# Performance work log

Measured on AMD Instinct MI355X. Metric: run time of the kernel, lower is better.

Reference implementation:

```python
import jax, jax.numpy as jnp
import numpy as np

B, T, D, H, E, O, A = 8192, 223, 7, 128, 50, 29, 9
IMPUTE_W, LABEL_W = 0.3, 1.0

def setup_inputs() -> dict:
    key = jax.random.key(0)
    ks = jax.random.split(key, 32)
    u = lambda k, shape, fan: jax.random.uniform(k, shape, jnp.float32, -1.0/np.sqrt(fan), 1.0/np.sqrt(fan))
    return {
        'values':    jax.random.normal(ks[0], (B, T, D), jnp.float32),
        'masks':     (jax.random.uniform(ks[1], (B, T, D)) < 0.8).astype(jnp.float32),
        'deltas':    jax.random.uniform(ks[2], (B, T, D), jnp.float32) * 5.0,
        'probs':     jax.nn.softmax(jax.random.normal(ks[3], (B, O), jnp.float32), axis=1),
        'ancillary': jax.random.normal(ks[4], (B, A), jnp.float32),
        'labels':    jax.random.randint(ks[5], (B,), 0, O, jnp.int32),
        'W_td_h': u(ks[6], (H, D), H),  'b_td_h': u(ks[7], (H,), H),
        'W_td_x': u(ks[8], (D, D), D),  'b_td_x': u(ks[9], (D,), D),
        'W_hist': u(ks[10], (D, H), H), 'b_hist': u(ks[11], (D,), H),
        'W_feat': u(ks[12], (D, D), D), 'b_feat': u(ks[13], (D,), D),
        'W_comb': u(ks[14], (D, 2*D), 2*D), 'b_comb': u(ks[15], (D,), 2*D),
        'W_ih': u(ks[16], (4*H, 2*D), H), 'W_hh': u(ks[17], (4*H, H), H),
        'b_ih': u(ks[18], (4*H,), H),     'b_hh': u(ks[19], (4*H,), H),
        'W_anc': u(ks[20], (E, A), A),    'b_anc': u(ks[21], (E,), A),
        'W_cat': u(ks[22], (H, H + E), H + E), 'b_cat': u(ks[23], (H,), H + E),
        'W_out': u(ks[24], (O, H), H),    'b_out': u(ks[25], (O,), H),
    }

def _rits_forward(values, masks, deltas, probs, ancillary,
                  W_td_h, b_td_h, W_td_x, b_td_x, W_hist, b_hist,
                  W_feat, b_feat, W_comb, b_comb, W_ih, W_hh, b_ih, b_hh,
                  W_anc, b_anc, W_cat, b_cat, W_out, b_out):
    Bn = values.shape[0]
    td_x_diag = jnp.diag(W_td_x)                     # diag=True decay uses only diagonal
    Wf = W_feat * (1.0 - jnp.eye(D, dtype=W_feat.dtype))

    def step(carry, xt):
        h, c, xl = carry
        x, m, d = xt                                  # each [B, D]
        gamma_h = jnp.exp(-jax.nn.relu(d @ W_td_h.T + b_td_h))   # [B, H]
        gamma_x = jnp.exp(-jax.nn.relu(d * td_x_diag + b_td_x))  # [B, D]
        h = h * gamma_h
        x_h = h @ W_hist.T + b_hist
        msum = jnp.sum(m) + 1e-5
        xl = xl + jnp.sum(jnp.abs(x - x_h) * m) / msum
        x_c = m * x + (1.0 - m) * x_h
        z_h = x_c @ Wf.T + b_feat
        xl = xl + jnp.sum(jnp.abs(x - z_h) * m) / msum
        alpha = jnp.concatenate([gamma_x, m], axis=1) @ W_comb.T + b_comb
        c_h = alpha * z_h + (1.0 - alpha) * x_h
        xl = xl + jnp.sum(jnp.abs(x - c_h) * m) / msum
        c_c = m * x + (1.0 - m) * c_h
        inputs = jnp.concatenate([c_c, m], axis=1)    # [B, 2D]
        gates = inputs @ W_ih.T + b_ih + h @ W_hh.T + b_hh  # [B, 4H]
        i, f, g, o = jnp.split(gates, 4, axis=1)
        c = jax.nn.sigmoid(f) * c + jax.nn.sigmoid(i) * jnp.tanh(g)
        h = jax.nn.sigmoid(o) * jnp.tanh(c)
        return (h, c, xl), c_c

    h0 = jnp.zeros((Bn, H), values.dtype)
    c0 = jnp.zeros((Bn, H), values.dtype)
    xs = (jnp.swapaxes(values, 0, 1), jnp.swapaxes(masks, 0, 1), jnp.swapaxes(deltas, 0, 1))
    (h, c, x_loss), imps = jax.lax.scan(step, (h0, c0, jnp.float32(0.0)), xs)
    imputations = jnp.swapaxes(imps, 0, 1)           # [B, T, D]

    x_loss = x_loss * IMPUTE_W
    anc = jax.nn.relu(ancillary @ W_anc.T + b_anc)
    h = jax.nn.relu(jnp.concatenate([h, anc], axis=1) @ W_cat.T + b_cat)
    y_h = jax.nn.softmax(h @ W_out.T + b_out, axis=1)
    y_loss = jnp.sum((y_h - probs) ** 2) / (Bn + 1e-5) * LABEL_W
    return x_loss, y_loss, x_loss + y_loss, y_h, imputations

def reference(values, masks, deltas, probs, ancillary, labels,
              W_td_h, b_td_h, W_td_x, b_td_x, W_hist, b_hist,
              W_feat, b_feat, W_comb, b_comb, W_ih, W_hh, b_ih, b_hh,
              W_anc, b_anc, W_cat, b_cat, W_out, b_out):
    x_loss, y_loss, loss, y_h, imputations = _rits_forward(
        values, masks, deltas, probs, ancillary,
        W_td_h, b_td_h, W_td_x, b_td_x, W_hist, b_hist,
        W_feat, b_feat, W_comb, b_comb, W_ih, W_hh, b_ih, b_hh,
        W_anc, b_anc, W_cat, b_cat, W_out, b_out)
    return (x_loss, y_loss, loss, y_h, imputations, labels)
```

## Files before the change

### kernel.cpp

```cpp
#include <hip/hip_runtime.h>
#include <math.h>

#define B_ 8192
#define T_ 223
#define D_ 7
#define H_ 128
#define G_ 512
#define E_ 50
#define O_ 29
#define A_ 9
#define TD_ (T_*D_)
#define NB 32
#define NTHR 512
#define MB 8

#define WS_MINV  0
#define WS_ACC   (WS_MINV + T_)
#define WS_WCATT (WS_ACC + 2)
#define WS_HFIN  (WS_WCATT + 178*H_)

#define OUT_YH  3
#define OUT_IMP (OUT_YH + B_*O_)
#define OUT_LAB (OUT_IMP + B_*T_*D_)

typedef __attribute__((ext_vector_type(8))) short short8;
typedef __attribute__((ext_vector_type(4))) float floatx4;
#define MFMA16(Av,Bv,Cv) __builtin_amdgcn_mfma_f32_16x16x32_bf16((Av),(Bv),(Cv),0,0,0)

__device__ __forceinline__ unsigned short f2bf(float f) {
    unsigned int u = __builtin_bit_cast(unsigned int, f);
    return (unsigned short)((u + 0x7FFFu + ((u >> 16) & 1u)) >> 16);
}
__device__ __forceinline__ float bf2f(unsigned short s) {
    unsigned int u = ((unsigned int)s) << 16;
    return __builtin_bit_cast(float, u);
}
__device__ __forceinline__ float rcp_(float x)  { return __builtin_amdgcn_rcpf(x); }
__device__ __forceinline__ float sigm(float x)  { return rcp_(1.f + __expf(-x)); }
__device__ __forceinline__ float tanh_(float x) { return 1.f - 2.f*rcp_(1.f + __expf(2.f*x)); }

__global__ void rits_prep(const float* __restrict__ W_cat, float* __restrict__ ws)
{
    int idx = blockIdx.x * 256 + threadIdx.x;
    if (idx < H_*178) {
        int j = idx / 178, k = idx - j*178;
        ws[WS_WCATT + k*H_ + j] = W_cat[idx];
    }
    if (idx < 2) ws[WS_ACC + idx] = 0.f;
}

__global__ void rits_msum(const float* __restrict__ masks, float* __restrict__ ws)
{
    const int t = blockIdx.x, tid = threadIdx.x;
    float s = 0.f;
    for (int i = tid; i < B_*D_; i += 256) {
        int b = i / D_, q = i - b*D_;
        s += masks[b*TD_ + t*D_ + q];
    }
    for (int off = 32; off > 0; off >>= 1) s += __shfl_down(s, off, 64);
    __shared__ float r[4];
    if ((tid & 63) == 0) r[tid >> 6] = s;
    __syncthreads();
    if (tid == 0) ws[WS_MINV + t] = 1.f / (r[0]+r[1]+r[2]+r[3] + 1e-5f);
}

__global__ __launch_bounds__(NTHR, 2) void rits_main(
    const float* __restrict__ values, const float* __restrict__ masks, const float* __restrict__ deltas,
    const float* __restrict__ W_td_h, const float* __restrict__ b_td_h,
    const float* __restrict__ W_td_x, const float* __restrict__ b_td_x,
    const float* __restrict__ W_hist, const float* __restrict__ b_hist,
    const float* __restrict__ W_feat, const float* __restrict__ b_feat,
    const float* __restrict__ W_comb, const float* __restrict__ b_comb,
    const float* __restrict__ W_ih, const float* __restrict__ W_hh,
    const float* __restrict__ b_ih, const float* __restrict__ b_hh,
    float* __restrict__ ws, float* __restrict__ out)
{
    __shared__ __attribute__((aligned(16))) unsigned short hbuf[NB*168];
    __shared__ __attribute__((aligned(16))) unsigned short dbuf[NB*72];
    __shared__ __attribute__((aligned(16))) unsigned short whis_lds[16*136];
    __shared__ float xs[NB*8], msh[NB*8], dsl[NB*8];
    __shared__ float xh_l[NB*8], xc_l[NB*8], gx_l[NB*8];
    __shared__ float bhist_l[8], tdx_l[8], btdx_l[8];
    __shared__ float impbuf[NB*16*7];
    __shared__ float red[8];

    const int tid  = threadIdx.x;
    const int b0   = blockIdx.x * NB;
    const int lane = tid & 63;
    const int w    = tid >> 6;
    const int quad = lane >> 4;
    const int l15  = lane & 15;

    for (int i = tid; i < NB*168; i += NTHR) hbuf[i] = 0;
    for (int i = tid; i < NB*72;  i += NTHR) dbuf[i] = 0;
    for (int i = tid; i < 16*136; i += NTHR) {
        int r = i / 136, c = i - r*136;
        whis_lds[i] = (r < 7 && c < 128) ? f2bf(W_hist[r*H_ + c]) : 0;
    }
    if (tid < 8) {
        bhist_l[tid] = (tid < 7) ? b_hist[tid] : 0.f;
        tdx_l[tid]   = (tid < 7) ? W_td_x[tid*D_ + tid] : 0.f;
        btdx_l[tid]  = (tid < 7) ? b_td_x[tid] : 0.f;
    }

    short8 whhf[4][4];
    short8 winf[4];
    short8 wtdf;
    float  biasg_r[4][4];
    float  btdh_r[4];
    {
        union UU { short8 v; unsigned short u[8]; } fr;
        #pragma unroll
        for (int c = 0; c < 4; ++c) {
            const int j = (c*8 + w)*16 + l15;
            #pragma unroll
            for (int s = 0; s < 4; ++s) {
                const float* p = W_hh + j*H_ + s*32 + quad*8;
                #pragma unroll
                for (int e = 0; e < 8; ++e) fr.u[e] = f2bf(p[e]);
                whhf[c][s] = fr.v;
            }
            #pragma unroll
            for (int e = 0; e < 8; ++e) {
                int k = quad*8 + e;
                fr.u[e] = (k < 14) ? f2bf(W_ih[j*14 + k]) : (unsigned short)0;
            }
            winf[c] = fr.v;
            #pragma unroll
            for (int r = 0; r < 4; ++r) {
                int jj = (c*8 + w)*16 + quad*4 + r;
                biasg_r[c][r] = b_ih[jj] + b_hh[jj];
            }
        }
        #pragma unroll
        for (int e = 0; e < 8; ++e) {
            int k = quad*8 + e;
            fr.u[e] = (k < 7) ? f2bf(W_td_h[(w*16 + l15)*D_ + k]) : (unsigned short)0;
        }
        wtdf = fr.v;
        #pragma unroll
        for (int r = 0; r < 4; ++r) btdh_r[r] = b_td_h[w*16 + quad*4 + r];
    }

    const bool ldr = (tid < NB*D_);
    const int  lb  = tid / D_, li = tid - (tid/D_)*D_;
    float wfr[7], wcr[14], bfr = 0.f, bcr = 0.f;
    if (ldr) {
        #pragma unroll
        for (int k = 0; k < 7; ++k)  wfr[k] = (k == li) ? 0.f : W_feat[li*D_ + k];
        #pragma unroll
        for (int k = 0; k < 14; ++k) wcr[k] = W_comb[li*14 + k];
        bfr = b_feat[li];  bcr = b_comb[li];
    }

    float c_st[2][4] = {{0,0,0,0},{0,0,0,0}};
    float lacc = 0.f;

    const long gbase = (long)(b0 + lb)*TD_ + li;
    float rx = 0.f, rm = 0.f, rd = 0.f;
    if (ldr) { rx = values[gbase]; rm = masks[gbase]; rd = deltas[gbase]; }

    const float* minv = ws + WS_MINV;

    for (int t = 0; t < T_; ++t) {
        if (ldr) { xs[lb*8+li] = rx; msh[lb*8+li] = rm; dsl[lb*8+li] = rd; }
        __syncthreads();
        if (ldr && t + 1 < T_) {
            const long g = gbase + (long)(t+1)*D_;
            rx = values[g]; rm = masks[g]; rd = deltas[g];
        }

        floatx4 acc[4][2];
        #pragma unroll
        for (int c = 0; c < 4; ++c)
            #pragma unroll
            for (int nt = 0; nt < 2; ++nt) {
                floatx4 a = { biasg_r[c][0], biasg_r[c][1], biasg_r[c][2], biasg_r[c][3] };
                acc[c][nt] = a;
            }
        floatx4 xh0 = {0,0,0,0}, xh1 = {0,0,0,0};
        #pragma unroll
        for (int s = 0; s < 4; ++s) {
            short8 hb0 = *(const short8*)&hbuf[l15*168       + s*32 + quad*8];
            short8 hb1 = *(const short8*)&hbuf[(16+l15)*168  + s*32 + quad*8];
            #pragma unroll
            for (int c = 0; c < 4; ++c) {
                acc[c][0] = MFMA16(whhf[c][s], hb0, acc[c][0]);
                acc[c][1] = MFMA16(whhf[c][s], hb1, acc[c][1]);
            }
            if (w == 7) {
                short8 wh = *(const short8*)&whis_lds[l15*136 + s*32 + quad*8];
                xh0 = MFMA16(wh, hb0, xh0);
                xh1 = MFMA16(wh, hb1, xh1);
            }
        }
        if (w == 7 && quad < 2) {
            #pragma unroll
            for (int nt = 0; nt < 2; ++nt) {
                const int b = nt*16 + l15;
                floatx4 xv = nt ? xh1 : xh0;
                #pragma unroll
                for (int r = 0; r < 4; ++r) {
                    const int i = quad*4 + r;
                    if (i < 7) {
                        float xhv = xv[r] + bhist_l[i];
                        float x = xs[b*8+i], m = msh[b*8+i], d = dsl[b*8+i];
                        xh_l[b*8+i] = xhv;
                        xc_l[b*8+i] = m*x + (1.f-m)*xhv;
                        gx_l[b*8+i] = __expf(-fmaxf(fmaf(d, tdx_l[i], btdx_l[i]), 0.f));
                    }
                }
            }
        }
        __syncthreads();

        if (ldr) {
            const int b = lb, i = li;
            const float invt = minv[t];
            const float x = xs[b*8+i], m = msh[b*8+i];
            float zh = bfr;
            #pragma unroll
            for (int k = 0; k < 7; ++k) zh = fmaf(wfr[k], xc_l[b*8+k], zh);
            float al = bcr;
            #pragma unroll
            for (int k = 0; k < 7; ++k) al = fmaf(wcr[k],   gx_l[b*8+k], al);
            #pragma unroll
            for (int k = 0; k < 7; ++k) al = fmaf(wcr[7+k], msh[b*8+k], al);
            const float xhv = xh_l[b*8+i];
            const float ch  = al*zh + (1.f-al)*xhv;
            const float cc  = m*x + (1.f-m)*ch;
            impbuf[(b*16 + (t & 15))*7 + i] = cc;
            hbuf[b*168 + 128 + i] = f2bf(cc);
            hbuf[b*168 + 135 + i] = f2bf(m);
            dbuf[b*72 + i] = f2bf(rd);
            lacc = fmaf((fabsf(x-xhv) + fabsf(x-zh) + fabsf(x-ch)) * m, invt, lacc);
        }
        __syncthreads();

        {
            short8 ib0 = *(const short8*)&hbuf[l15*168      + 128 + quad*8];
            short8 ib1 = *(const short8*)&hbuf[(16+l15)*168 + 128 + quad*8];
            #pragma unroll
            for (int c = 0; c < 4; ++c) {
                acc[c][0] = MFMA16(winf[c], ib0, acc[c][0]);
                acc[c][1] = MFMA16(winf[c], ib1, acc[c][1]);
            }
        }
        floatx4 g0 = {0,0,0,0}, g1 = {0,0,0,0};
        const bool dec = (t + 1 < T_);
        if (dec) {
            short8 df0 = *(const short8*)&dbuf[l15*72      + quad*8];
            short8 df1 = *(const short8*)&dbuf[(16+l15)*72 + quad*8];
            floatx4 z = {0,0,0,0};
            g0 = MFMA16(wtdf, df0, z);
            g1 = MFMA16(wtdf, df1, z);
        }
        #pragma unroll
        for (int nt = 0; nt < 2; ++nt) {
            const int b = nt*16 + l15;
            floatx4 gg = nt ? g1 : g0;
            #pragma unroll
            for (int r = 0; r < 4; ++r) {
                float ig = acc[0][nt][r], fg = acc[1][nt][r];
                float gv = acc[2][nt][r], og = acc[3][nt][r];
                float cn = sigm(fg)*c_st[nt][r] + sigm(ig)*tanh_(gv);
                c_st[nt][r] = cn;
                float hn = sigm(og)*tanh_(cn);
                if (dec) hn *= __expf(-fmaxf(gg[r] + btdh_r[r], 0.f));
                hbuf[b*168 + w*16 + quad*4 + r] = f2bf(hn);
            }
        }

        if ((t & 15) == 15 || t == T_ - 1) {
            const int t0 = t & ~15;
            const int b  = tid >> 4, c16 = tid & 15;
            if (t0 + c16 <= t) {
                float* gp = out + (size_t)OUT_IMP + (size_t)(b0+b)*TD_ + (size_t)(t0+c16)*D_;
                const float* lp = &impbuf[(b*16 + c16)*7];
                #pragma unroll
                for (int e = 0; e < 7; ++e) gp[e] = lp[e];
            }
        }
    }
    __syncthreads();

    for (int off = 32; off > 0; off >>= 1) lacc += __shfl_down(lacc, off, 64);
    if ((tid & 63) == 0) red[tid >> 6] = lacc;
    __syncthreads();
    if (tid == 0) {
        float s = 0.f;
        #pragma unroll
        for (int q = 0; q < 8; ++q) s += red[q];
        atomicAdd(&ws[WS_ACC], s);
    }
    for (int i = tid; i < NB*H_; i += NTHR) {
        int b = i >> 7, j = i & 127;
        ws[WS_HFIN + (size_t)(b0+b)*H_ + j] = bf2f(hbuf[b*168 + j]);
    }
}

__global__ __launch_bounds__(128) void rits_head(
    const float* __restrict__ probs, const float* __restrict__ ancillary, const int* __restrict__ labels,
    const float* __restrict__ W_anc, const float* __restrict__ b_anc,
    const float* __restrict__ b_cat,
    const float* __restrict__ W_out, const float* __restrict__ b_out,
    float* __restrict__ ws, float* __restrict__ out)
{
    __shared__ float hb[MB*H_];
    __shared__ float ancl[MB*52];
    __shared__ float hc[MB*H_];
    __shared__ float lg[MB*32];
    __shared__ float smx[MB], sinv[MB], ysum[MB];
    __shared__ float sq[MB*32];
    const int tid = threadIdx.x;
    const int bb0 = blockIdx.x * MB;

    for (int i = tid; i < MB*H_; i += 128) hb[i] = ws[WS_HFIN + (size_t)bb0*H_ + i];
    for (int i = tid; i < MB*E_; i += 128) {
        int b = i / E_, e = i - b*E_;
        float s = b_anc[e];
        #pragma unroll
        for (int a = 0; a < A_; ++a) s = fmaf(ancillary[(bb0+b)*A_ + a], W_anc[e*A_ + a], s);
        ancl[b*52+e] = fmaxf(s, 0.f);
    }
    __syncthreads();
    {
        const int j = tid;
        float s[MB];
        #pragma unroll
        for (int b = 0; b < MB; ++b) s[b] = b_cat[j];
        const float* wc = ws + WS_WCATT;
        for (int k = 0; k < H_; ++k) {
            float wv = wc[k*H_ + j];
            #pragma unroll
            for (int b = 0; b < MB; ++b) s[b] = fmaf(hb[b*H_+k], wv, s[b]);
        }
        for (int k = 0; k < E_; ++k) {
            float wv = wc[(H_+k)*H_ + j];
            #pragma unroll
            for (int b = 0; b < MB; ++b) s[b] = fmaf(ancl[b*52+k], wv, s[b]);
        }
        #pragma unroll
        for (int b = 0; b < MB; ++b) hc[b*H_+j] = fmaxf(s[b], 0.f);
    }
    __syncthreads();
    for (int i = tid; i < MB*O_; i += 128) {
        int b = i / O_, o = i - b*O_;
        float s = b_out[o];
        for (int k = 0; k < H_; ++k) s = fmaf(hc[b*H_+k], W_out[o*H_+k], s);
        lg[b*32+o] = s;
    }
    __syncthreads();
    if (tid < MB) {
        float mx = -1e30f;
        for (int o = 0; o < O_; ++o) mx = fmaxf(mx, lg[tid*32+o]);
        float se = 0.f;
        for (int o = 0; o < O_; ++o) se += __expf(lg[tid*32+o] - mx);
        smx[tid] = mx; sinv[tid] = 1.f / se;
    }
    __syncthreads();
    for (int i = tid; i < MB*O_; i += 128) {
        int b = i / O_, o = i - b*O_;
        float y = __expf(lg[b*32+o] - smx[b]) * sinv[b];
        out[OUT_YH + (size_t)(bb0+b)*O_ + o] = y;
        float d = y - probs[(size_t)(bb0+b)*O_ + o];
        sq[b*32+o] = d*d;
    }
    __syncthreads();
    if (tid < MB) {
        float s = 0.f;
        for (int o = 0; o < O_; ++o) s += sq[tid*32+o];
        ysum[tid] = s;
        out[OUT_LAB + bb0 + tid] = (float)labels[bb0 + tid];
    }
    __syncthreads();
    if (tid == 0) {
        float s = 0.f;
        #pragma unroll
        for (int b = 0; b < MB; ++b) s += ysum[b];
        atomicAdd(&ws[WS_ACC+1], s);
    }
}

__global__ void rits_fin(const float* __restrict__ ws, float* __restrict__ out)
{
    if (blockIdx.x == 0 && threadIdx.x == 0) {
        float xl = ws[WS_ACC] * 0.3f;
        float yl = ws[WS_ACC+1] * (1.0f / (8192.0f + 1e-5f));
        out[0] = xl; out[1] = yl; out[2] = xl + yl;
    }
}

extern "C" void kernel_launch(void* const* d_in, const int* in_sizes, int n_in,
                              void* d_out, int out_size, void* d_ws, size_t ws_size,
                              hipStream_t stream)
{
    const float* values = (const float*)d_in[0];
    const float* masks  = (const float*)d_in[1];
    const float* deltas = (const float*)d_in[2];
    const float* probs  = (const float*)d_in[3];
    const float* ancil  = (const float*)d_in[4];
    const int*   labels = (const int*)  d_in[5];
    const float* W_td_h = (const float*)d_in[6];
    const float* b_td_h = (const float*)d_in[7];
    const float* W_td_x = (const float*)d_in[8];
    const float* b_td_x = (const float*)d_in[9];
    const float* W_hist = (const float*)d_in[10];
    const float* b_hist = (const float*)d_in[11];
    const float* W_feat = (const float*)d_in[12];
    const float* b_feat = (const float*)d_in[13];
    const float* W_comb = (const float*)d_in[14];
    const float* b_comb = (const float*)d_in[15];
    const float* W_ih   = (const float*)d_in[16];
    const float* W_hh   = (const float*)d_in[17];
    const float* b_ih   = (const float*)d_in[18];
    const float* b_hh   = (const float*)d_in[19];
    const float* W_anc  = (const float*)d_in[20];
    const float* b_anc  = (const float*)d_in[21];
    const float* W_cat  = (const float*)d_in[22];
    const float* b_cat  = (const float*)d_in[23];
    const float* W_out  = (const float*)d_in[24];
    const float* b_out  = (const float*)d_in[25];
    float* ws  = (float*)d_ws;
    float* out = (float*)d_out;

    hipLaunchKernelGGL(rits_prep, dim3((H_*178 + 255)/256), dim3(256), 0, stream, W_cat, ws);
    hipLaunchKernelGGL(rits_msum, dim3(T_), dim3(256), 0, stream, masks, ws);
    hipLaunchKernelGGL(rits_main, dim3(B_/NB), dim3(NTHR), 0, stream,
                       values, masks, deltas, W_td_h, b_td_h, W_td_x, b_td_x,
                       W_hist, b_hist, W_feat, b_feat, W_comb, b_comb,
                       W_ih, W_hh, b_ih, b_hh, ws, out);
    hipLaunchKernelGGL(rits_head, dim3(B_/MB), dim3(128), 0, stream,
                       probs, ancil, labels, W_anc, b_anc, b_cat, W_out, b_out, ws, out);
    hipLaunchKernelGGL(rits_fin, dim3(1), dim3(1), 0, stream, ws, out);
}
```

Measured before the change: 1.041 ms.

## Halve batch per block to double blocks, and parallelize mask-sum reduction

The main recurrent kernel now processes 16 batch rows per block instead of 32. That doubles the grid to 512 blocks and raises launch bounds to 4 blocks per CU, so more CUs get work and the latency-bound serial time loop is better hidden. Each wave now issues half the MFMAs per step but repeats the weight loads and barriers per block. The mask-sum kernel is restructured into 7x128 blocks with coalesced column reads and atomic accumulation, and the reciprocal moves into the main kernel. This adds atomics and nondeterministic summation order.

```diff
diff --git a/kernel.cpp b/kernel.cpp
--- a/kernel.cpp
+++ b/kernel.cpp
@@ -10,9 +10,10 @@
 #define O_ 29
 #define A_ 9
 #define TD_ (T_*D_)
-#define NB 32
+#define NB 16
 #define NTHR 512
 #define MB 8
+#define MS_BG 128
 
 #define WS_MINV  0
 #define WS_ACC   (WS_MINV + T_)
@@ -46,25 +47,37 @@
         int j = idx / 178, k = idx - j*178;
         ws[WS_WCATT + k*H_ + j] = W_cat[idx];
     }
+    if (idx < T_) ws[WS_MINV + idx] = 0.f;
     if (idx < 2) ws[WS_ACC + idx] = 0.f;
 }
 
 __global__ void rits_msum(const float* __restrict__ masks, float* __restrict__ ws)
 {
-    const int t = blockIdx.x, tid = threadIdx.x;
+    const int tc = blockIdx.x % 7;
+    const int bg = blockIdx.x / 7;
+    const int t0 = tc * 32;
+    const int nt = (t0 + 32 <= T_) ? 32 : (T_ - t0);
+    const int ncol = nt * D_;
+    const int tid = threadIdx.x;
+    __shared__ float sums[224];
     float s = 0.f;
-    for (int i = tid; i < B_*D_; i += 256) {
-        int b = i / D_, q = i - b*D_;
-        s += masks[b*TD_ + t*D_ + q];
-    }
-    for (int off = 32; off > 0; off >>= 1) s += __shfl_down(s, off, 64);
-    __shared__ float r[4];
-    if ((tid & 63) == 0) r[tid >> 6] = s;
-    __syncthreads();
-    if (tid == 0) ws[WS_MINV + t] = 1.f / (r[0]+r[1]+r[2]+r[3] + 1e-5f);
-}
-
-__global__ __launch_bounds__(NTHR, 2) void rits_main(
+    if (tid < ncol) {
+        const int bpg = B_ / MS_BG;
+        const float* p = masks + (size_t)bg * bpg * TD_ + (size_t)t0 * D_ + tid;
+        #pragma unroll 4
+        for (int b = 0; b < bpg; ++b) s += p[(size_t)b * TD_];
+    }
+    if (tid < 224) sums[tid] = (tid < ncol) ? s : 0.f;
+    __syncthreads();
+    if (tid < 32) {
+        float r = 0.f;
+        #pragma unroll
+        for (int q = 0; q < 7; ++q) r += sums[tid*7 + q];
+        if (t0 + tid < T_) atomicAdd(&ws[WS_MINV + t0 + tid], r);
+    }
+}
+
+__global__ __launch_bounds__(NTHR, 4) void rits_main(
     const float* __restrict__ values, const float* __restrict__ masks, const float* __restrict__ deltas,
     const float* __restrict__ W_td_h, const float* __restrict__ b_td_h,
     const float* __restrict__ W_td_x, const float* __restrict__ b_td_x,
@@ -153,14 +166,14 @@
         bfr = b_feat[li];  bcr = b_comb[li];
     }
 
-    float c_st[2][4] = {{0,0,0,0},{0,0,0,0}};
+    float c_st[4] = {0,0,0,0};
     float lacc = 0.f;
 
     const long gbase = (long)(b0 + lb)*TD_ + li;
     float rx = 0.f, rm = 0.f, rd = 0.f;
     if (ldr) { rx = values[gbase]; rm = masks[gbase]; rd = deltas[gbase]; }
 
-    const float* minv = ws + WS_MINV;
+    const float* msums = ws + WS_MINV;
 
     for (int t = 0; t < T_; ++t) {
         if (ldr) { xs[lb*8+li] = rx; msh[lb*8+li] = rm; dsl[lb*8+li] = rd; }
@@ -170,45 +183,35 @@
             rx = values[g]; rm = masks[g]; rd = deltas[g];
         }
 
-        floatx4 acc[4][2];
-        #pragma unroll
-        for (int c = 0; c < 4; ++c)
-            #pragma unroll
-            for (int nt = 0; nt < 2; ++nt) {
-                floatx4 a = { biasg_r[c][0], biasg_r[c][1], biasg_r[c][2], biasg_r[c][3] };
-                acc[c][nt] = a;
-            }
-        floatx4 xh0 = {0,0,0,0}, xh1 = {0,0,0,0};
+        floatx4 acc[4];
+        #pragma unroll
+        for (int c = 0; c < 4; ++c) {
+            floatx4 a = { biasg_r[c][0], biasg_r[c][1], biasg_r[c][2], biasg_r[c][3] };
+            acc[c] = a;
+        }
+        floatx4 xh0 = {0,0,0,0};
         #pragma unroll
         for (int s = 0; s < 4; ++s) {
-            short8 hb0 = *(const short8*)&hbuf[l15*168       + s*32 + quad*8];
-            short8 hb1 = *(const short8*)&hbuf[(16+l15)*168  + s*32 + quad*8];
-            #pragma unroll
-            for (int c = 0; c < 4; ++c) {
-                acc[c][0] = MFMA16(whhf[c][s], hb0, acc[c][0]);
-                acc[c][1] = MFMA16(whhf[c][s], hb1, acc[c][1]);
-            }
+            short8 hb0 = *(const short8*)&hbuf[l15*168 + s*32 + quad*8];
+            #pragma unroll
+            for (int c = 0; c < 4; ++c)
+                acc[c] = MFMA16(whhf[c][s], hb0, acc[c]);
             if (w == 7) {
                 short8 wh = *(const short8*)&whis_lds[l15*136 + s*32 + quad*8];
                 xh0 = MFMA16(wh, hb0, xh0);
-                xh1 = MFMA16(wh, hb1, xh1);
             }
         }
         if (w == 7 && quad < 2) {
-            #pragma unroll
-            for (int nt = 0; nt < 2; ++nt) {
-                const int b = nt*16 + l15;
-                floatx4 xv = nt ? xh1 : xh0;
-                #pragma unroll
-                for (int r = 0; r < 4; ++r) {
-                    const int i = quad*4 + r;
-                    if (i < 7) {
-                        float xhv = xv[r] + bhist_l[i];
-                        float x = xs[b*8+i], m = msh[b*8+i], d = dsl[b*8+i];
-                        xh_l[b*8+i] = xhv;
-                        xc_l[b*8+i] = m*x + (1.f-m)*xhv;
-                        gx_l[b*8+i] = __expf(-fmaxf(fmaf(d, tdx_l[i], btdx_l[i]), 0.f));
-                    }
+            const int b = l15;
+            #pragma unroll
+            for (int r = 0; r < 4; ++r) {
+                const int i = quad*4 + r;
+                if (i < 7) {
+                    float xhv = xh0[r] + bhist_l[i];
+                    float x = xs[b*8+i], m = msh[b*8+i], d = dsl[b*8+i];
+                    xh_l[b*8+i] = xhv;
+                    xc_l[b*8+i] = m*x + (1.f-m)*xhv;
+                    gx_l[b*8+i] = __expf(-fmaxf(fmaf(d, tdx_l[i], btdx_l[i]), 0.f));
                 }
             }
         }
@@ -216,7 +219,7 @@
 
         if (ldr) {
             const int b = lb, i = li;
-            const float invt = minv[t];
+            const float invt = 1.0f / (msums[t] + 1e-5f);
             const float x = xs[b*8+i], m = msh[b*8+i];
             float zh = bfr;
             #pragma unroll
@@ -238,35 +241,28 @@
         __syncthreads();
 
         {
-            short8 ib0 = *(const short8*)&hbuf[l15*168      + 128 + quad*8];
-            short8 ib1 = *(const short8*)&hbuf[(16+l15)*168 + 128 + quad*8];
-            #pragma unroll
-            for (int c = 0; c < 4; ++c) {
-                acc[c][0] = MFMA16(winf[c], ib0, acc[c][0]);
-                acc[c][1] = MFMA16(winf[c], ib1, acc[c][1]);
-            }
-        }
-        floatx4 g0 = {0,0,0,0}, g1 = {0,0,0,0};
+            short8 ib0 = *(const short8*)&hbuf[l15*168 + 128 + quad*8];
+            #pragma unroll
+            for (int c = 0; c < 4; ++c)
+                acc[c] = MFMA16(winf[c], ib0, acc[c]);
+        }
+        floatx4 g0 = {0,0,0,0};
         const bool dec = (t + 1 < T_);
         if (dec) {
-            short8 df0 = *(const short8*)&dbuf[l15*72      + quad*8];
-            short8 df1 = *(const short8*)&dbuf[(16+l15)*72 + quad*8];
+            short8 df0 = *(const short8*)&dbuf[l15*72 + quad*8];
             floatx4 z = {0,0,0,0};
             g0 = MFMA16(wtdf, df0, z);
-            g1 = MFMA16(wtdf, df1, z);
-        }
-        #pragma unroll
-        for (int nt = 0; nt < 2; ++nt) {
-            const int b = nt*16 + l15;
-            floatx4 gg = nt ? g1 : g0;
+        }
+        {
+            const int b = l15;
             #pragma unroll
             for (int r = 0; r < 4; ++r) {
-                float ig = acc[0][nt][r], fg = acc[1][nt][r];
-                float gv = acc[2][nt][r], og = acc[3][nt][r];
-                float cn = sigm(fg)*c_st[nt][r] + sigm(ig)*tanh_(gv);
-                c_st[nt][r] = cn;
+                float ig = acc[0][r], fg = acc[1][r];
+                float gv = acc[2][r], og = acc[3][r];
+                float cn = sigm(fg)*c_st[r] + sigm(ig)*tanh_(gv);
+                c_st[r] = cn;
                 float hn = sigm(og)*tanh_(cn);
-                if (dec) hn *= __expf(-fmaxf(gg[r] + btdh_r[r], 0.f));
+                if (dec) hn *= __expf(-fmaxf(g0[r] + btdh_r[r], 0.f));
                 hbuf[b*168 + w*16 + quad*4 + r] = f2bf(hn);
             }
         }
@@ -274,7 +270,7 @@
         if ((t & 15) == 15 || t == T_ - 1) {
             const int t0 = t & ~15;
             const int b  = tid >> 4, c16 = tid & 15;
-            if (t0 + c16 <= t) {
+            if (b < NB && t0 + c16 <= t) {
                 float* gp = out + (size_t)OUT_IMP + (size_t)(b0+b)*TD_ + (size_t)(t0+c16)*D_;
                 const float* lp = &impbuf[(b*16 + c16)*7];
                 #pragma unroll
@@ -425,7 +421,7 @@
     float* out = (float*)d_out;
 
     hipLaunchKernelGGL(rits_prep, dim3((H_*178 + 255)/256), dim3(256), 0, stream, W_cat, ws);
-    hipLaunchKernelGGL(rits_msum, dim3(T_), dim3(256), 0, stream, masks, ws);
+    hipLaunchKernelGGL(rits_msum, dim3(7*MS_BG), dim3(256), 0, stream, masks, ws);
     hipLaunchKernelGGL(rits_main, dim3(B_/NB), dim3(NTHR), 0, stream,
                        values, masks, deltas, W_td_h, b_td_h, W_td_x, b_td_x,
                        W_hist, b_hist, W_feat, b_feat, W_comb, b_comb,
```

New measurement: 3.526 ms. +238.8%, slower.

## Restructure mask-sum reduction, move decay MFMA earlier, and pack hidden-state stores

Applied to the files above, without the earlier changes.

The mask-sum kernel changes from one block per timestep with strided gathers to blocks that cover a contiguous time-chunk and batch-group. These blocks read coalesced columns and atomically accumulate raw sums, and the reciprocal is now computed in the main loop. In the main kernel, the delta bf16 write moves before the first barrier, so the decay MFMA can be issued before the imputation scalar phase and overlap with it. The per-element bf16 hidden-state LDS writes are packed into one 8-byte store. Float atomics make the loss summation order nondeterministic.

```diff
diff --git a/kernel.cpp b/kernel.cpp
--- a/kernel.cpp
+++ b/kernel.cpp
@@ -5,7 +5,6 @@
 #define T_ 223
 #define D_ 7
 #define H_ 128
-#define G_ 512
 #define E_ 50
 #define O_ 29
 #define A_ 9
@@ -13,6 +12,7 @@
 #define NB 32
 #define NTHR 512
 #define MB 8
+#define MS_BG 128
 
 #define WS_MINV  0
 #define WS_ACC   (WS_MINV + T_)
@@ -46,22 +46,34 @@
         int j = idx / 178, k = idx - j*178;
         ws[WS_WCATT + k*H_ + j] = W_cat[idx];
     }
+    if (idx < T_) ws[WS_MINV + idx] = 0.f;
     if (idx < 2) ws[WS_ACC + idx] = 0.f;
 }
 
 __global__ void rits_msum(const float* __restrict__ masks, float* __restrict__ ws)
 {
-    const int t = blockIdx.x, tid = threadIdx.x;
+    const int tc = blockIdx.x % 7;
+    const int bg = blockIdx.x / 7;
+    const int t0 = tc * 32;
+    const int nt = (t0 + 32 <= T_) ? 32 : (T_ - t0);
+    const int ncol = nt * D_;
+    const int tid = threadIdx.x;
+    __shared__ float sums[224];
     float s = 0.f;
-    for (int i = tid; i < B_*D_; i += 256) {
-        int b = i / D_, q = i - b*D_;
-        s += masks[b*TD_ + t*D_ + q];
-    }
-    for (int off = 32; off > 0; off >>= 1) s += __shfl_down(s, off, 64);
-    __shared__ float r[4];
-    if ((tid & 63) == 0) r[tid >> 6] = s;
-    __syncthreads();
-    if (tid == 0) ws[WS_MINV + t] = 1.f / (r[0]+r[1]+r[2]+r[3] + 1e-5f);
+    if (tid < ncol) {
+        const int bpg = B_ / MS_BG;
+        const float* p = masks + (size_t)bg * bpg * TD_ + (size_t)t0 * D_ + tid;
+        #pragma unroll 4
+        for (int b = 0; b < bpg; ++b) s += p[(size_t)b * TD_];
+    }
+    if (tid < 224) sums[tid] = (tid < ncol) ? s : 0.f;
+    __syncthreads();
+    if (tid < 32) {
+        float r = 0.f;
+        #pragma unroll
+        for (int q = 0; q < 7; ++q) r += sums[tid*7 + q];
+        if (t0 + tid < T_) atomicAdd(&ws[WS_MINV + t0 + tid], r);
+    }
 }
 
 __global__ __launch_bounds__(NTHR, 2) void rits_main(
@@ -160,14 +172,17 @@
     float rx = 0.f, rm = 0.f, rd = 0.f;
     if (ldr) { rx = values[gbase]; rm = masks[gbase]; rd = deltas[gbase]; }
 
-    const float* minv = ws + WS_MINV;
+    const float* msums = ws + WS_MINV;
 
     for (int t = 0; t < T_; ++t) {
         if (ldr) { xs[lb*8+li] = rx; msh[lb*8+li] = rm; dsl[lb*8+li] = rd; }
         __syncthreads();
-        if (ldr && t + 1 < T_) {
-            const long g = gbase + (long)(t+1)*D_;
-            rx = values[g]; rm = masks[g]; rd = deltas[g];
+        if (ldr) {
+            if (t + 1 < T_) {
+                const long g = gbase + (long)(t+1)*D_;
+                rx = values[g]; rm = masks[g]; rd = deltas[g];
+            }
+            dbuf[lb*72 + li] = f2bf(rd);
         }
 
         floatx4 acc[4][2];
@@ -214,38 +229,6 @@
         }
         __syncthreads();
 
-        if (ldr) {
-            const int b = lb, i = li;
-            const float invt = minv[t];
-            const float x = xs[b*8+i], m = msh[b*8+i];
-            float zh = bfr;
-            #pragma unroll
-            for (int k = 0; k < 7; ++k) zh = fmaf(wfr[k], xc_l[b*8+k], zh);
-            float al = bcr;
-            #pragma unroll
-            for (int k = 0; k < 7; ++k) al = fmaf(wcr[k],   gx_l[b*8+k], al);
-            #pragma unroll
-            for (int k = 0; k < 7; ++k) al = fmaf(wcr[7+k], msh[b*8+k], al);
-            const float xhv = xh_l[b*8+i];
-            const float ch  = al*zh + (1.f-al)*xhv;
-            const float cc  = m*x + (1.f-m)*ch;
-            impbuf[(b*16 + (t & 15))*7 + i] = cc;
-            hbuf[b*168 + 128 + i] = f2bf(cc);
-            hbuf[b*168 + 135 + i] = f2bf(m);
-            dbuf[b*72 + i] = f2bf(rd);
-            lacc = fmaf((fabsf(x-xhv) + fabsf(x-zh) + fabsf(x-ch)) * m, invt, lacc);
-        }
-        __syncthreads();
-
-        {
-            short8 ib0 = *(const short8*)&hbuf[l15*168      + 128 + quad*8];
-            short8 ib1 = *(const short8*)&hbuf[(16+l15)*168 + 128 + quad*8];
-            #pragma unroll
-            for (int c = 0; c < 4; ++c) {
-                acc[c][0] = MFMA16(winf[c], ib0, acc[c][0]);
-                acc[c][1] = MFMA16(winf[c], ib1, acc[c][1]);
-            }
-        }
         floatx4 g0 = {0,0,0,0}, g1 = {0,0,0,0};
         const bool dec = (t + 1 < T_);
         if (dec) {
@@ -255,10 +238,43 @@
             g0 = MFMA16(wtdf, df0, z);
             g1 = MFMA16(wtdf, df1, z);
         }
+
+        if (ldr) {
+            const int b = lb, i = li;
+            const float invt = rcp_(msums[t] + 1e-5f);
+            const float x = xs[b*8+i], m = msh[b*8+i];
+            float zh = bfr;
+            #pragma unroll
+            for (int k = 0; k < 7; ++k) zh = fmaf(wfr[k], xc_l[b*8+k], zh);
+            float al = bcr;
+            #pragma unroll
+            for (int k = 0; k < 7; ++k) al = fmaf(wcr[k],   gx_l[b*8+k], al);
+            #pragma unroll
+            for (int k = 0; k < 7; ++k) al = fmaf(wcr[7+k], msh[b*8+k], al);
+            const float xhv = xh_l[b*8+i];
+            const float ch  = al*zh + (1.f-al)*xhv;
+            const float cc  = m*x + (1.f-m)*ch;
+            impbuf[(b*16 + (t & 15))*7 + i] = cc;
+            hbuf[b*168 + 128 + i] = f2bf(cc);
+            hbuf[b*168 + 135 + i] = f2bf(m);
+            lacc = fmaf((fabsf(x-xhv) + fabsf(x-zh) + fabsf(x-ch)) * m, invt, lacc);
+        }
+        __syncthreads();
+
+        {
+            short8 ib0 = *(const short8*)&hbuf[l15*168      + 128 + quad*8];
+            short8 ib1 = *(const short8*)&hbuf[(16+l15)*168 + 128 + quad*8];
+            #pragma unroll
+            for (int c = 0; c < 4; ++c) {
+                acc[c][0] = MFMA16(winf[c], ib0, acc[c][0]);
+                acc[c][1] = MFMA16(winf[c], ib1, acc[c][1]);
+            }
+        }
         #pragma unroll
         for (int nt = 0; nt < 2; ++nt) {
             const int b = nt*16 + l15;
             floatx4 gg = nt ? g1 : g0;
+            float hnv[4];
             #pragma unroll
             for (int r = 0; r < 4; ++r) {
                 float ig = acc[0][nt][r], fg = acc[1][nt][r];
@@ -267,8 +283,12 @@
                 c_st[nt][r] = cn;
                 float hn = sigm(og)*tanh_(cn);
                 if (dec) hn *= __expf(-fmaxf(gg[r] + btdh_r[r], 0.f));
-                hbuf[b*168 + w*16 + quad*4 + r] = f2bf(hn);
-            }
+                hnv[r] = hn;
+            }
+            uint2 pk;
+            pk.x = (unsigned)f2bf(hnv[0]) | ((unsigned)f2bf(hnv[1]) << 16);
+            pk.y = (unsigned)f2bf(hnv[2]) | ((unsigned)f2bf(hnv[3]) << 16);
+            *(uint2*)&hbuf[b*168 + w*16 + quad*4] = pk;
         }
 
         if ((t & 15) == 15 || t == T_ - 1) {
@@ -425,7 +445,7 @@
     float* out = (float*)d_out;
 
     hipLaunchKernelGGL(rits_prep, dim3((H_*178 + 255)/256), dim3(256), 0, stream, W_cat, ws);
-    hipLaunchKernelGGL(rits_msum, dim3(T_), dim3(256), 0, stream, masks, ws);
+    hipLaunchKernelGGL(rits_msum, dim3(7*MS_BG), dim3(256), 0, stream, masks, ws);
     hipLaunchKernelGGL(rits_main, dim3(B_/NB), dim3(NTHR), 0, stream,
                        values, masks, deltas, W_td_h, b_td_h, W_td_x, b_td_x,
                        W_hist, b_hist, W_feat, b_feat, W_comb, b_comb,
```

New measurement: 933.8 us. 10.3% less time.
